# Kernel tuning notes

Hardware: AMD Instinct MI355X
Metric: run time of the kernel (lower is better)

Reference implementation:

```python
import jax, jax.numpy as jnp
from jax import lax
import numpy as np

B, W, V, E, H = 512, 40, 12000, 512, 512


def setup_inputs() -> dict:
    key = jax.random.key(0)
    ks = jax.random.split(key, 9)
    s = 0.05
    ques_vec = jax.random.randint(ks[0], (B, W), 0, V + 1)          # token ids, 0 = pad
    ques_len = jax.random.randint(ks[1], (B,), 1, W + 1)             # valid lengths in [1, W]
    lookup_W = jax.random.normal(ks[2], (E, V), jnp.float32) * s     # nn.Linear(vocab, emb).weight
    wih0 = jax.random.normal(ks[3], (2, 4 * H, E), jnp.float32) * s  # [dir, 4H, in]
    whh0 = jax.random.normal(ks[4], (2, 4 * H, H), jnp.float32) * s
    b0 = jax.random.normal(ks[5], (2, 2, 4 * H), jnp.float32) * s    # [dir, {b_ih,b_hh}, 4H]
    wih1 = jax.random.normal(ks[6], (2, 4 * H, 2 * H), jnp.float32) * s
    whh1 = jax.random.normal(ks[7], (2, 4 * H, H), jnp.float32) * s
    b1 = jax.random.normal(ks[8], (2, 2, 4 * H), jnp.float32) * s
    return {"ques_vec": ques_vec, "ques_len": ques_len, "lookup_W": lookup_W,
            "wih0": wih0, "whh0": whh0, "b0": b0,
            "wih1": wih1, "whh1": whh1, "b1": b1}


def _lstm_dir(x, wih, whh, b, reverse):
    # x: [B, T, D]; PyTorch gate order i, f, g, o
    Hc = whh.shape[1]
    xg = jnp.einsum('btd,gd->btg', x, wih) + b[0] + b[1]  # [B, T, 4H]
    xs = jnp.swapaxes(xg, 0, 1)                            # [T, B, 4H]
    if reverse:
        xs = xs[::-1]

    def step(carry, g_t):
        h, c = carry
        g = g_t + h @ whh.T
        i, f, gg, o = jnp.split(g, 4, axis=-1)
        c = jax.nn.sigmoid(f) * c + jax.nn.sigmoid(i) * jnp.tanh(gg)
        h = jax.nn.sigmoid(o) * jnp.tanh(c)
        return (h, c), h

    h0 = jnp.zeros((x.shape[0], Hc), x.dtype)
    _, hs = lax.scan(step, (h0, h0), xs)
    if reverse:
        hs = hs[::-1]
    return jnp.swapaxes(hs, 0, 1)  # [B, T, H]


def _bilstm(x, wih, whh, b):
    fwd = _lstm_dir(x, wih[0], whh[0], b[0], False)
    bwd = _lstm_dir(x, wih[1], whh[1], b[1], True)
    return jnp.concatenate([fwd, bwd], axis=-1)  # [B, T, 2H]


def reference(ques_vec, ques_len, lookup_W, wih0, whh0, b0, wih1, whh1, b1):
    # one-hot over vocab+1 with column 0 dropped == gather with id 0 -> zero vector
    table = jnp.concatenate([jnp.zeros((1, E), lookup_W.dtype), lookup_W.T], axis=0)  # [V+1, E]
    emb = jnp.tanh(table[ques_vec])          # [B, W, E] (dropout=0 -> identity)
    h = _bilstm(emb, wih0, whh0, b0)         # layer 0
    h = _bilstm(h, wih1, whh1, b1)           # layer 1 -> [B, W, 2H]
    # scatter-mask bmm == select hidden state at timestep ques_len-1
    idx = (ques_len - 1)[:, None, None]
    return jnp.take_along_axis(h, idx, axis=1).reshape(ques_vec.shape[0], -1)  # [B, 2H]
```

## Files before the change

### kernel.cpp

```cpp
#include <hip/hip_runtime.h>
#include <hip/hip_bf16.h>
#include <stdint.h>

#define NB 512
#define NW 40
#define NE 512
#define NH 512
#define NV 12000
#define G4 2048

typedef unsigned short u16;
typedef unsigned int u32;
typedef unsigned long long u64;
typedef __attribute__((ext_vector_type(8))) short short8;
typedef __attribute__((ext_vector_type(4))) float f32x4;

__device__ __forceinline__ unsigned short f2bf(float f) {
  unsigned int u = __float_as_uint(f);
  u += 0x7FFF + ((u >> 16) & 1);
  return (unsigned short)(u >> 16);
}
__device__ __forceinline__ float bf2f(unsigned short b) {
  return __uint_as_float(((unsigned int)b) << 16);
}
__device__ __forceinline__ float loadIn(const void* p, long i, int bf) {
  return bf ? bf2f(((const u16*)p)[i]) : ((const float*)p)[i];
}
__device__ __forceinline__ float fast_tanh(float x) {
  float ax = __builtin_fabsf(x);
  float t = 1.f - 2.f * __builtin_amdgcn_rcpf(__expf(ax + ax) + 1.f);
  return __builtin_copysignf(t, x);
}
__device__ __forceinline__ float sigm(float x) {
  return __builtin_amdgcn_rcpf(1.f + __expf(-x));
}

__global__ void detect_kernel(const u16* p, int* flag) {
  __shared__ int cnt;
  int i = threadIdx.x;
  if (i == 0) cnt = 0;
  __syncthreads();
  unsigned short u = p[2 * (i * 1001)];
  int e = (u >> 7) & 0xFF;
  if (e >= 100 && e <= 126) atomicAdd(&cnt, 1);
  __syncthreads();
  if (i == 0) *flag = (cnt >= 32) ? 1 : 0;
}

__global__ void table_kernel(const void* lookup, const int* flag, u16* tableT) {
  __shared__ float tile[64][65];
  int bf = *flag;
  int v0 = blockIdx.x * 64, e0 = blockIdx.y * 64;
  int tx = threadIdx.x, ty = threadIdx.y;
#pragma unroll
  for (int r = 0; r < 16; ++r) {
    int e = r * 4 + ty, v = tx;
    if (v0 + v < NV)
      tile[e][v] = tanhf(loadIn(lookup, (long)(e0 + e) * NV + v0 + v, bf));
  }
  __syncthreads();
#pragma unroll
  for (int r = 0; r < 16; ++r) {
    int v = r * 4 + ty, e = tx;
    if (v0 + v < NV)
      tableT[(long)(v0 + v) * NE + e0 + e] = f2bf(tile[e][v]);
  }
}

__global__ void pack_kernel(const void* wih0, const void* whh0, const void* b0,
                            const void* wih1, const void* whh1, const void* b1,
                            const int* flag, u16* Wc0, u16* Wc1, float* bsum,
                            u16* G) {
  const long N0 = 2L * G4 * 1024, N1 = 2L * G4 * 1536;
  const long NB2 = 2L * 2 * G4;
  long idx = (long)blockIdx.x * 256 + threadIdx.x;
  int bf = *flag;
  if (idx < N0) {
    int d = (int)(idx / (G4 * 1024));
    int rem = (int)(idx % (long)(G4 * 1024));
    int g = rem / 1024, k = rem % 1024;
    float v = (k < 512) ? loadIn(wih0, ((long)d * G4 + g) * 512 + k, bf)
                        : loadIn(whh0, ((long)d * G4 + g) * 512 + (k - 512), bf);
    Wc0[idx] = f2bf(v);
  } else if (idx < N0 + N1) {
    long i2 = idx - N0;
    int d = (int)(i2 / (G4 * 1536));
    int rem = (int)(i2 % (long)(G4 * 1536));
    int g = rem / 1536, k = rem % 1536;
    float v = (k < 1024) ? loadIn(wih1, ((long)d * G4 + g) * 1024 + k, bf)
                         : loadIn(whh1, ((long)d * G4 + g) * 512 + (k - 1024), bf);
    Wc1[i2] = f2bf(v);
  } else if (idx < N0 + N1 + NB2) {
    long i3 = idx - N0 - N1;
    int layer = (int)(i3 / (2 * G4));
    int d = (int)((i3 / G4) & 1);
    int g = (int)(i3 % G4);
    const void* bb = layer ? b1 : b0;
    float v = loadIn(bb, (long)d * 2 * G4 + g, bf) +
              loadIn(bb, (long)d * 2 * G4 + G4 + g, bf);
    bsum[i3] = v;
  } else if (idx < N0 + N1 + NB2 + 4096) {
    int n = (int)(idx - N0 - N1 - NB2);
    int d = n >> 11, loc = n & 2047;
    int colb = loc >> 7, rr = loc & 127;
    int jn = rr >> 2, g = rr & 3;
    int grow = g * 512 + colb * 32 + jn;
    float v = loadIn(b0, (long)d * 2 * G4 + grow, bf) +
              loadIn(b0, (long)d * 2 * G4 + G4 + grow, bf);
    G[n] = f2bf(v);
  }
}

__global__ void zero_bar(unsigned int* bar) {
  bar[blockIdx.x * 256 + threadIdx.x] = 0u;
}

__global__ __launch_bounds__(256, 3) void g_gemm(
    const u16* __restrict__ tableT, const u16* __restrict__ Wc,
    const float* __restrict__ bsumL, u16* __restrict__ G) {
  __shared__ __align__(16) char lds[32768];
  const int tid = threadIdx.x;
  const int lane = tid & 63, wv = tid >> 6;
  const int wm = wv & 1, wn = wv >> 1;
  const int col = lane & 15, quad = lane >> 4;
  const int bx = blockIdx.x >> 5;
  const int by = blockIdx.x & 31;
  const int tb0 = bx * 128;
  const int d = by >> 4, colb = by & 15, j0 = colb * 32;

  f32x4 zero = {0.f, 0.f, 0.f, 0.f};
  f32x4 acc[4][4];
#pragma unroll
  for (int i = 0; i < 4; ++i)
#pragma unroll
    for (int j = 0; j < 4; ++j) acc[i][j] = zero;

  for (int it = 0; it < 8; ++it) {
    int k0 = it << 6;
#pragma unroll
    for (int p = 0; p < 8; ++p) {
      int c = p * 256 + tid;
      const u16* gsrc;
      if (c < 1024) {
        int r = c >> 3, sl = c & 7;
        int kk = k0 + ((sl * 8) ^ ((r & 7) << 3));
        gsrc = tableT + (long)(tb0 + r) * 512 + kk;
      } else {
        int cb = c - 1024;
        int r = cb >> 3, sl = cb & 7;
        int kk = k0 + ((sl * 8) ^ ((r & 7) << 3));
        int grow = (r >> 5) * 512 + j0 + (r & 31);
        gsrc = Wc + ((long)d * G4 + grow) * 1024 + kk;
      }
      __builtin_amdgcn_global_load_lds(
          (const __attribute__((address_space(1))) void*)(const void*)gsrc,
          (__attribute__((address_space(3))) void*)(lds + p * 4096 + wv * 1024),
          16, 0, 0);
    }
    __syncthreads();
    const u16* As = (const u16*)lds;
    const u16* Bs = (const u16*)(lds + 16384);
#pragma unroll
    for (int ks = 0; ks < 2; ++ks) {
      short8 afr[4], bfr[4];
#pragma unroll
      for (int mf = 0; mf < 4; ++mf) {
        int rm = wm * 64 + mf * 16 + col;
        int sl = (ks * 32 + quad * 8) ^ ((rm & 7) << 3);
        afr[mf] = *(const short8*)(As + rm * 64 + sl);
      }
#pragma unroll
      for (int nf = 0; nf < 4; ++nf) {
        int br = wn * 64 + nf * 16 + col;
        int sl = (ks * 32 + quad * 8) ^ ((br & 7) << 3);
        bfr[nf] = *(const short8*)(Bs + br * 64 + sl);
      }
#pragma unroll
      for (int mf = 0; mf < 4; ++mf)
#pragma unroll
        for (int nf = 0; nf < 4; ++nf)
          acc[mf][nf] = __builtin_amdgcn_mfma_f32_16x16x32_bf16(
              afr[mf], bfr[nf], acc[mf][nf], 0, 0, 0);
    }
    __syncthreads();
  }

  float bias[4];
#pragma unroll
  for (int nf = 0; nf < 4; ++nf) {
    int n = wn * 64 + nf * 16 + col;
    bias[nf] = bsumL[d * G4 + (n >> 5) * 512 + j0 + (n & 31)];
  }
#pragma unroll
  for (int mf = 0; mf < 4; ++mf)
#pragma unroll
    for (int nf = 0; nf < 4; ++nf) {
      int n = wn * 64 + nf * 16 + col;
      int g = n >> 5, jn = n & 31;
#pragma unroll
      for (int r = 0; r < 4; ++r) {
        int m = wm * 64 + mf * 16 + quad * 4 + r;
        int v = tb0 + m;
        if (v < NV)
          G[(long)(v + 1) * 4096 + ((d * 16 + colb) << 7) + jn * 4 + g] =
              f2bf(acc[mf][nf][r] + bias[nf]);
      }
    }
}

__global__ __launch_bounds__(256, 3) void xg_gemm(
    const u16* __restrict__ X, int Kx, int Kfull, const u16* __restrict__ Wc,
    const float* __restrict__ bsumL, u16* __restrict__ xg) {
  __shared__ __align__(16) char lds[32768];
  const int tid = threadIdx.x;
  const int lane = tid & 63, wv = tid >> 6;
  const int wm = wv & 1, wn = wv >> 1;
  const int col = lane & 15, quad = lane >> 4;
  const int s = blockIdx.x >> 5, w = blockIdx.x & 31;
  const int bx = (s % 40) * 4 + (w & 3);
  const int by = (s / 40) * 8 + (w >> 2);
  const int tb0 = bx * 128;
  const int d = by >> 4, colb = by & 15, j0 = colb * 32;

  f32x4 zero = {0.f, 0.f, 0.f, 0.f};
  f32x4 acc[4][4];
#pragma unroll
  for (int i = 0; i < 4; ++i)
#pragma unroll
    for (int j = 0; j < 4; ++j) acc[i][j] = zero;

  const int iters = Kx >> 6;
  for (int it = 0; it < iters; ++it) {
    int k0 = it << 6;
#pragma unroll
    for (int p = 0; p < 8; ++p) {
      int c = p * 256 + tid;
      const u16* gsrc;
      if (c < 1024) {
        int r = c >> 3, sl = c & 7;
        int kk = k0 + ((sl * 8) ^ ((r & 7) << 3));
        gsrc = X + (long)(tb0 + r) * Kx + kk;
      } else {
        int cb = c - 1024;
        int r = cb >> 3, sl = cb & 7;
        int kk = k0 + ((sl * 8) ^ ((r & 7) << 3));
        int grow = (r >> 5) * 512 + j0 + (r & 31);
        gsrc = Wc + ((long)d * G4 + grow) * Kfull + kk;
      }
      __builtin_amdgcn_global_load_lds(
          (const __attribute__((address_space(1))) void*)(const void*)gsrc,
          (__attribute__((address_space(3))) void*)(lds + p * 4096 + wv * 1024),
          16, 0, 0);
    }
    __syncthreads();
    const u16* As = (const u16*)lds;
    const u16* Bs = (const u16*)(lds + 16384);
#pragma unroll
    for (int ks = 0; ks < 2; ++ks) {
      short8 afr[4], bfr[4];
#pragma unroll
      for (int mf = 0; mf < 4; ++mf) {
        int rm = wm * 64 + mf * 16 + col;
        int sl = (ks * 32 + quad * 8) ^ ((rm & 7) << 3);
        afr[mf] = *(const short8*)(As + rm * 64 + sl);
      }
#pragma unroll
      for (int nf = 0; nf < 4; ++nf) {
        int br = wn * 64 + nf * 16 + col;
        int sl = (ks * 32 + quad * 8) ^ ((br & 7) << 3);
        bfr[nf] = *(const short8*)(Bs + br * 64 + sl);
      }
#pragma unroll
      for (int mf = 0; mf < 4; ++mf)
#pragma unroll
        for (int nf = 0; nf < 4; ++nf)
          acc[mf][nf] = __builtin_amdgcn_mfma_f32_16x16x32_bf16(
              afr[mf], bfr[nf], acc[mf][nf], 0, 0, 0);
    }
    __syncthreads();
  }

  float bias[4];
#pragma unroll
  for (int nf = 0; nf < 4; ++nf) {
    int n = wn * 64 + nf * 16 + col;
    bias[nf] = bsumL[d * G4 + (n >> 5) * 512 + j0 + (n & 31)];
  }
#pragma unroll
  for (int mf = 0; mf < 4; ++mf)
#pragma unroll
    for (int nf = 0; nf < 4; ++nf) {
      int n = wn * 64 + nf * 16 + col;
      int g = n >> 5, jn = n & 31;
#pragma unroll
      for (int r = 0; r < 4; ++r) {
        int m = wm * 64 + mf * 16 + quad * 4 + r;
        int tb = tb0 + m, t = tb >> 9, b = tb & 511;
        long oi = ((((long)t * 2 + d) * 16 + colb) * 512 + b) * 128 + jn * 4 + g;
        xg[oi] = f2bf(acc[mf][nf][r] + bias[nf]);
      }
    }
}

__global__ __launch_bounds__(256, 1) void lstm_pers(
    const u16* __restrict__ xg, const int* __restrict__ qv,
    const u16* __restrict__ Wc, int Kfull, int Kx, u16* __restrict__ hbuf,
    u16* __restrict__ h0cat, void* __restrict__ outp,
    const int* __restrict__ qlen, const int* __restrict__ flag,
    unsigned int* bar, int layer) {
  __shared__ __align__(16) char lds[163840];
  const int tid = threadIdx.x;
  const int lane = tid & 63, wv = tid >> 6;
  const int wm = wv & 1, wn = wv >> 1;
  const int col = lane & 15, quad = lane >> 4;
  const int l = blockIdx.x;
  const int colid = l & 31, mi = l >> 5;
  const int colb = colid & 15, j0 = colb * 32, d = colid >> 4;
  const int m0 = mi * 64;
  const int gid = l >> 4;

#pragma unroll
  for (int p = 0; p < 24; ++p) {
    int c = p * 256 + tid;
    int cc = c >> 10, row = (c >> 3) & 127, sl = c & 7;
    int grow = (row >> 5) * 512 + j0 + (row & 31);
    int gk = Kx + 128 + cc * 64 + ((sl * 8) ^ ((row & 7) << 3));
    const u16* gsrc = Wc + ((long)d * G4 + grow) * Kfull + gk;
    __builtin_amdgcn_global_load_lds(
        (const __attribute__((address_space(1))) void*)(const void*)gsrc,
        (__attribute__((address_space(3))) void*)(lds + p * 4096 + wv * 1024),
        16, 0, 0);
  }
  const u16* WhhB = (const u16*)lds;
  char* hstg = lds + 98304;
  u16* hLDS = (u16*)hstg;

  short8 breg[4][4];
#pragma unroll
  for (int g = 0; g < 4; ++g) {
    int grow = g * 512 + j0 + wn * 16 + col;
    const u16* wp = Wc + ((long)d * G4 + grow) * Kfull + Kx;
#pragma unroll
    for (int c4 = 0; c4 < 4; ++c4)
      breg[g][c4] = *(const short8*)(wp + c4 * 32 + quad * 8);
  }

  float creg[2][4];
#pragma unroll
  for (int i = 0; i < 2; ++i)
#pragma unroll
    for (int r = 0; r < 4; ++r) creg[i][r] = 0.f;
  const int isbf = *flag;
  f32x4 zero = {0.f, 0.f, 0.f, 0.f};

  __syncthreads();

#pragma unroll 1
  for (int t = 0; t < NW; ++t) {
    const int tq = d ? (NW - 1 - t) : t;

    ushort4 xgv[2][4];
    if (layer == 0) {
#pragma unroll
      for (int mf = 0; mf < 2; ++mf)
#pragma unroll
        for (int r = 0; r < 4; ++r) {
          int m = wm * 32 + mf * 16 + quad * 4 + r;
          int q = qv[(m0 + m) * NW + tq];
          xgv[mf][r] = *(const ushort4*)(xg + (long)q * 4096 +
                                         ((d * 16 + colb) << 7) +
                                         (wn * 16 + col) * 4);
        }
    } else {
      const u16* xgt =
          xg + ((((long)tq * 2 + d) * 16 + colb) * 512 + m0) * 128;
#pragma unroll
      for (int mf = 0; mf < 2; ++mf)
#pragma unroll
        for (int r = 0; r < 4; ++r) {
          int m = wm * 32 + mf * 16 + quad * 4 + r;
          xgv[mf][r] = *(const ushort4*)(xgt + m * 128 + (wn * 16 + col) * 4);
        }
    }

    f32x4 acc[2][4];
#pragma unroll
    for (int i = 0; i < 2; ++i)
#pragma unroll
      for (int j = 0; j < 4; ++j) acc[i][j] = zero;

    if (t > 0) {
      if (wv == 0) {
        u32* sp = bar + gid * 16 + (lane & 15);
        while (__ballot((int)(__hip_atomic_load(sp, __ATOMIC_RELAXED,
                                                __HIP_MEMORY_SCOPE_AGENT) <
                              (u32)t)))
          __builtin_amdgcn_s_sleep(1);
      }
      __syncthreads();

      const u16* hp =
          hbuf + ((t - 1) & 1) * (2L * NB * NH) + ((long)d * NB + m0) * NH;
#pragma unroll
      for (int p = 0; p < 16; ++p) {
        int c = p * 256 + tid;
        int row = c >> 6, slot = c & 63;
        int kk = (slot >> 3) * 64 + (((slot & 7) * 8) ^ ((row & 7) << 3));
        const u16* gsrc = hp + (long)row * NH + kk;
        __builtin_amdgcn_global_load_lds(
            (const __attribute__((address_space(1))) void*)(const void*)gsrc,
            (__attribute__((address_space(3))) void*)(hstg + p * 4096 +
                                                      wv * 1024),
            16, 0, 16 );
      }
      __syncthreads();

      const u16* As = (const u16*)hstg;
#pragma unroll
      for (int ks = 0; ks < 16; ++ks) {
        const int ksub = ks * 32 + quad * 8;
        short8 afr[2];
#pragma unroll
        for (int mf = 0; mf < 2; ++mf) {
          int rm = wm * 32 + mf * 16 + col;
          afr[mf] = *(const short8*)(As + rm * 512 + (ksub & ~63) +
                                     ((ksub & 63) ^ ((rm & 7) << 3)));
        }
#pragma unroll
        for (int g = 0; g < 4; ++g) {
          short8 bfr;
          if (ks < 4) {
            bfr = breg[g][ks];
          } else {
            int br = g * 32 + wn * 16 + col;
            int kp = ksub - 128;
            bfr = *(const short8*)(WhhB + (kp >> 6) * 8192 + br * 64 +
                                   ((kp & 63) ^ ((br & 7) << 3)));
          }
#pragma unroll
          for (int mf = 0; mf < 2; ++mf)
            acc[mf][g] = __builtin_amdgcn_mfma_f32_16x16x32_bf16(
                afr[mf], bfr, acc[mf][g], 0, 0, 0);
        }
      }
      __syncthreads();
    }

#pragma unroll
    for (int mf = 0; mf < 2; ++mf)
#pragma unroll
      for (int r = 0; r < 4; ++r) {
        int m = wm * 32 + mf * 16 + quad * 4 + r;
        const u16* xv = (const u16*)&xgv[mf][r];
        float gi = acc[mf][0][r] + bf2f(xv[0]);
        float gf = acc[mf][1][r] + bf2f(xv[1]);
        float gg = acc[mf][2][r] + bf2f(xv[2]);
        float go = acc[mf][3][r] + bf2f(xv[3]);
        float si = sigm(gi);
        float sf = sigm(gf);
        float so = sigm(go);
        float cn = sf * creg[mf][r] + si * fast_tanh(gg);
        float h = so * fast_tanh(cn);
        creg[mf][r] = cn;
        hLDS[m * 32 + wn * 16 + col] = f2bf(h);
        if (layer == 1 && !isbf) {
          int bg = m0 + m;
          if (qlen[bg] - 1 == tq)
            ((float*)outp)[(long)bg * (2 * NH) + d * NH + j0 + wn * 16 + col] =
                h;
        }
      }
    __syncthreads();

    u16* hnxt = hbuf + (t & 1) * (2L * NB * NH);
    u32 hw[4];
    int bgp[4], jgp[4];
#pragma unroll
    for (int p = 0; p < 4; ++p) {
      int c = p * 256 + tid;
      int m = c >> 4, pr = c & 15;
      hw[p] = ((const u32*)hLDS)[m * 16 + pr];
      bgp[p] = m0 + m;
      jgp[p] = j0 + pr * 2;
      __hip_atomic_store(
          (u32*)(hnxt + ((long)d * NB + bgp[p]) * NH + jgp[p]), hw[p],
          __ATOMIC_RELAXED, __HIP_MEMORY_SCOPE_AGENT);
    }

    if (t < NW - 1) {
      __syncthreads();
      if (tid == 0)
        __hip_atomic_store(bar + gid * 16 + colb, (u32)(t + 1),
                           __ATOMIC_RELAXED, __HIP_MEMORY_SCOPE_AGENT);
    }

#pragma unroll
    for (int p = 0; p < 4; ++p) {
      if (layer == 0) {
        *(u32*)(h0cat + ((long)tq * NB + bgp[p]) * (2 * NH) + d * NH +
                jgp[p]) = hw[p];
      } else if (isbf && qlen[bgp[p]] - 1 == tq) {
        *(u32*)((u16*)outp + (long)bgp[p] * (2 * NH) + d * NH + jgp[p]) =
            hw[p];
      }
    }
  }
}

extern "C" void kernel_launch(void* const* d_in, const int* in_sizes, int n_in,
                              void* d_out, int out_size, void* d_ws,
                              size_t ws_size, hipStream_t stream) {
  const int* qv = (const int*)d_in[0];
  const int* ql = (const int*)d_in[1];
  const void* lookup = d_in[2];
  const void* wih0 = d_in[3];
  const void* whh0 = d_in[4];
  const void* b0 = d_in[5];
  const void* wih1 = d_in[6];
  const void* whh1 = d_in[7];
  const void* b1 = d_in[8];

  char* ws = (char*)d_ws;
  size_t off = 0;
  int* flag = (int*)ws;                 off += 256;
  unsigned int* bar = (unsigned int*)(ws + off); off += 8192;
  float* bsum = (float*)(ws + off);     off += 2L * 2 * G4 * 4;
  u16* Wc0 = (u16*)(ws + off);          off += 2L * G4 * 1024 * 2;
  u16* Wc1 = (u16*)(ws + off);          off += 2L * G4 * 1536 * 2;
  u16* hbuf = (u16*)(ws + off);         off += 2L * 2 * NB * NH * 2;
  u16* h0cat = (u16*)(ws + off);        off += (size_t)NW * NB * 2 * NH * 2;
  u16* xg = (u16*)(ws + off);           off += (size_t)NW * 2 * 16 * 512 * 128 * 2;
  u16* tableT = h0cat;
  u16* G = xg;

  detect_kernel<<<1, 64, 0, stream>>>((const u16*)lookup, flag);
  table_kernel<<<dim3(188, 8), dim3(64, 4), 0, stream>>>(lookup, flag, tableT);
  {
    long total = 2L * G4 * 1024 + 2L * G4 * 1536 + 2L * 2 * G4 + 4096;
    int blocks = (int)((total + 255) / 256);
    pack_kernel<<<blocks, 256, 0, stream>>>(wih0, whh0, b0, wih1, whh1, b1,
                                            flag, Wc0, Wc1, bsum, G);
  }

  g_gemm<<<94 * 32, 256, 0, stream>>>(tableT, Wc0, bsum, G);
  zero_bar<<<8, 256, 0, stream>>>(bar);
  lstm_pers<<<256, 256, 0, stream>>>(G, qv, Wc0, 1024, 512, hbuf, h0cat,
                                     d_out, ql, flag, bar, 0);
  xg_gemm<<<5120, 256, 0, stream>>>(h0cat, 1024, 1536, Wc1, bsum + 2 * G4, xg);
  zero_bar<<<8, 256, 0, stream>>>(bar);
  lstm_pers<<<256, 256, 0, stream>>>(xg, qv, Wc1, 1536, 1024, hbuf, h0cat,
                                     d_out, ql, flag, bar, 1);
}
```

Baseline: 832.5 us.

## Rewrite layer-1 input GEMM with 256x256 tiles and double-buffered LDS prefetch

The layer-1 input-projection GEMM now uses 512-thread blocks, each computing a 256x256 output tile. Global-to-LDS loads for the next K tile are double-buffered and interleaved with MFMA work, and s_setprio raises priority around the MFMA issue. Barrier zeroing is folded into pack_kernel, and each layer gets its own barrier region, which removes two tiny kernel launches. The cost is heavy LDS use (128KB) and one block per CU, which lowers occupancy. The loop is hardcoded to 16 K tiles, which assumes Kx=1024.

```diff
diff --git a/kernel.cpp b/kernel.cpp
--- a/kernel.cpp
+++ b/kernel.cpp
@@ -70,7 +70,7 @@
 __global__ void pack_kernel(const void* wih0, const void* whh0, const void* b0,
                             const void* wih1, const void* whh1, const void* b1,
                             const int* flag, u16* Wc0, u16* Wc1, float* bsum,
-                            u16* G) {
+                            u16* G, unsigned int* bar) {
   const long N0 = 2L * G4 * 1024, N1 = 2L * G4 * 1536;
   const long NB2 = 2L * 2 * G4;
   long idx = (long)blockIdx.x * 256 + threadIdx.x;
@@ -108,11 +108,9 @@
     float v = loadIn(b0, (long)d * 2 * G4 + grow, bf) +
               loadIn(b0, (long)d * 2 * G4 + G4 + grow, bf);
     G[n] = f2bf(v);
-  }
-}
-
-__global__ void zero_bar(unsigned int* bar) {
-  bar[blockIdx.x * 256 + threadIdx.x] = 0u;
+  } else if (idx < N0 + N1 + NB2 + 4096 + 512) {
+    bar[(int)(idx - N0 - N1 - NB2 - 4096)] = 0u;
+  }
 }
 
 __global__ __launch_bounds__(256, 3) void g_gemm(
@@ -208,98 +206,132 @@
     }
 }
 
-__global__ __launch_bounds__(256, 3) void xg_gemm(
+__global__ __launch_bounds__(512, 1) void xg_gemm(
     const u16* __restrict__ X, int Kx, int Kfull, const u16* __restrict__ Wc,
     const float* __restrict__ bsumL, u16* __restrict__ xg) {
-  __shared__ __align__(16) char lds[32768];
+  __shared__ __align__(16) char lds[131072];
   const int tid = threadIdx.x;
   const int lane = tid & 63, wv = tid >> 6;
-  const int wm = wv & 1, wn = wv >> 1;
+  const int wm = wv >> 2, wn = wv & 3;
   const int col = lane & 15, quad = lane >> 4;
-  const int s = blockIdx.x >> 5, w = blockIdx.x & 31;
-  const int bx = (s % 40) * 4 + (w & 3);
-  const int by = (s / 40) * 8 + (w >> 2);
-  const int tb0 = bx * 128;
-  const int d = by >> 4, colb = by & 15, j0 = colb * 32;
+  const int w = blockIdx.x & 15, s = blockIdx.x >> 4;
+  const int bx = (s % 20) * 4 + (w & 3);
+  const int by = (s / 20) * 4 + (w >> 2);
+  const int tb0 = bx * 256;
+  const int d = by >> 3;
 
   f32x4 zero = {0.f, 0.f, 0.f, 0.f};
-  f32x4 acc[4][4];
-#pragma unroll
-  for (int i = 0; i < 4; ++i)
+  f32x4 acc[8][4];
+#pragma unroll
+  for (int i = 0; i < 8; ++i)
 #pragma unroll
     for (int j = 0; j < 4; ++j) acc[i][j] = zero;
 
-  const int iters = Kx >> 6;
-  for (int it = 0; it < iters; ++it) {
-    int k0 = it << 6;
-#pragma unroll
-    for (int p = 0; p < 8; ++p) {
-      int c = p * 256 + tid;
+  const int nkt = Kx >> 6;
+
+  auto stage = [&](int kt, int j) {
+    char* dst = lds + (kt & 1) * 65536 + ((j >> 1) * 32768) + ((j & 1) * 16384);
+#pragma unroll
+    for (int i = 0; i < 2; ++i) {
+      int idx = i * 512 + tid;
+      int row = idx >> 3, sl = idx & 7;
+      int rr = (j & 1) * 128 + row;
+      int kk = kt * 64 + ((sl * 8) ^ ((rr & 7) << 3));
       const u16* gsrc;
-      if (c < 1024) {
-        int r = c >> 3, sl = c & 7;
-        int kk = k0 + ((sl * 8) ^ ((r & 7) << 3));
-        gsrc = X + (long)(tb0 + r) * Kx + kk;
+      if (j < 2) {
+        gsrc = X + (long)(tb0 + rr) * Kx + kk;
       } else {
-        int cb = c - 1024;
-        int r = cb >> 3, sl = cb & 7;
-        int kk = k0 + ((sl * 8) ^ ((r & 7) << 3));
-        int grow = (r >> 5) * 512 + j0 + (r & 31);
+        int n2 = (by & 7) * 256 + rr;
+        int grow = ((n2 & 127) >> 5) * 512 + (n2 >> 7) * 32 + (n2 & 31);
         gsrc = Wc + ((long)d * G4 + grow) * Kfull + kk;
       }
       __builtin_amdgcn_global_load_lds(
           (const __attribute__((address_space(1))) void*)(const void*)gsrc,
-          (__attribute__((address_space(3))) void*)(lds + p * 4096 + wv * 1024),
+          (__attribute__((address_space(3))) void*)(dst + i * 8192 + wv * 1024),
           16, 0, 0);
     }
-    __syncthreads();
-    const u16* As = (const u16*)lds;
-    const u16* Bs = (const u16*)(lds + 16384);
-#pragma unroll
-    for (int ks = 0; ks < 2; ++ks) {
-      short8 afr[4], bfr[4];
+  };
+
+#pragma unroll
+  for (int j = 0; j < 4; ++j) stage(0, j);
+
+#pragma unroll 1
+  for (int kt = 0; kt < 16; ++kt) {
+    if (kt + 1 < 16) {
+      stage(kt + 1, 0);
+      asm volatile("s_waitcnt vmcnt(2)" ::: "memory");
+    } else {
+      asm volatile("s_waitcnt vmcnt(0)" ::: "memory");
+    }
+    __builtin_amdgcn_sched_barrier(0);
+    __builtin_amdgcn_s_barrier();
+    __builtin_amdgcn_sched_barrier(0);
+
+    const u16* As = (const u16*)(lds + (kt & 1) * 65536);
+    const u16* Bs = As + 16384;
+
+#pragma unroll
+    for (int q = 0; q < 4; ++q) {
+      const int qr = q >> 1, qc = q & 1;
+      short8 afr[4][2], bfr[2][2];
 #pragma unroll
       for (int mf = 0; mf < 4; ++mf) {
-        int rm = wm * 64 + mf * 16 + col;
-        int sl = (ks * 32 + quad * 8) ^ ((rm & 7) << 3);
-        afr[mf] = *(const short8*)(As + rm * 64 + sl);
-      }
-#pragma unroll
-      for (int nf = 0; nf < 4; ++nf) {
-        int br = wn * 64 + nf * 16 + col;
-        int sl = (ks * 32 + quad * 8) ^ ((br & 7) << 3);
-        bfr[nf] = *(const short8*)(Bs + br * 64 + sl);
-      }
+        int rm = wm * 128 + qr * 64 + mf * 16 + col;
+#pragma unroll
+        for (int ks = 0; ks < 2; ++ks) {
+          int ksub = ks * 32 + quad * 8;
+          afr[mf][ks] =
+              *(const short8*)(As + rm * 64 + (ksub ^ ((rm & 7) << 3)));
+        }
+      }
+#pragma unroll
+      for (int nf = 0; nf < 2; ++nf) {
+        int bn = wn * 64 + qc * 32 + nf * 16 + col;
+#pragma unroll
+        for (int ks = 0; ks < 2; ++ks) {
+          int ksub = ks * 32 + quad * 8;
+          bfr[nf][ks] =
+              *(const short8*)(Bs + bn * 64 + (ksub ^ ((bn & 7) << 3)));
+        }
+      }
+      if (q > 0 && kt + 1 < 16) stage(kt + 1, q);
+      __builtin_amdgcn_s_setprio(1);
 #pragma unroll
       for (int mf = 0; mf < 4; ++mf)
 #pragma unroll
-        for (int nf = 0; nf < 4; ++nf)
-          acc[mf][nf] = __builtin_amdgcn_mfma_f32_16x16x32_bf16(
-              afr[mf], bfr[nf], acc[mf][nf], 0, 0, 0);
-    }
-    __syncthreads();
-  }
-
-  float bias[4];
+        for (int nf = 0; nf < 2; ++nf)
+#pragma unroll
+          for (int ks = 0; ks < 2; ++ks)
+            acc[qr * 4 + mf][qc * 2 + nf] =
+                __builtin_amdgcn_mfma_f32_16x16x32_bf16(
+                    afr[mf][ks], bfr[nf][ks], acc[qr * 4 + mf][qc * 2 + nf], 0,
+                    0, 0);
+      __builtin_amdgcn_s_setprio(0);
+      __builtin_amdgcn_sched_barrier(0);
+      __builtin_amdgcn_s_barrier();
+      __builtin_amdgcn_sched_barrier(0);
+    }
+  }
+
 #pragma unroll
   for (int nf = 0; nf < 4; ++nf) {
-    int n = wn * 64 + nf * 16 + col;
-    bias[nf] = bsumL[d * G4 + (n >> 5) * 512 + j0 + (n & 31)];
-  }
-#pragma unroll
-  for (int mf = 0; mf < 4; ++mf)
-#pragma unroll
-    for (int nf = 0; nf < 4; ++nf) {
-      int n = wn * 64 + nf * 16 + col;
-      int g = n >> 5, jn = n & 31;
+    int nc = wn * 64 + nf * 16 + col;
+    int n2 = (by & 7) * 256 + nc;
+    int colb = n2 >> 7, nq = n2 & 127;
+    int g = nq >> 5, jn = nq & 31;
+    float bias = bsumL[d * G4 + g * 512 + colb * 32 + jn];
+#pragma unroll
+    for (int mf = 0; mf < 8; ++mf) {
 #pragma unroll
       for (int r = 0; r < 4; ++r) {
-        int m = wm * 64 + mf * 16 + quad * 4 + r;
+        int m = wm * 128 + mf * 16 + quad * 4 + r;
         int tb = tb0 + m, t = tb >> 9, b = tb & 511;
-        long oi = ((((long)t * 2 + d) * 16 + colb) * 512 + b) * 128 + jn * 4 + g;
-        xg[oi] = f2bf(acc[mf][nf][r] + bias[nf]);
-      }
-    }
+        long oi =
+            ((((long)t * 2 + d) * 16 + colb) * 512 + b) * 128 + jn * 4 + g;
+        xg[oi] = f2bf(acc[mf][nf][r] + bias);
+      }
+    }
+  }
 }
 
 __global__ __launch_bounds__(256, 1) void lstm_pers(
@@ -536,18 +568,16 @@
   detect_kernel<<<1, 64, 0, stream>>>((const u16*)lookup, flag);
   table_kernel<<<dim3(188, 8), dim3(64, 4), 0, stream>>>(lookup, flag, tableT);
   {
-    long total = 2L * G4 * 1024 + 2L * G4 * 1536 + 2L * 2 * G4 + 4096;
+    long total = 2L * G4 * 1024 + 2L * G4 * 1536 + 2L * 2 * G4 + 4096 + 512;
     int blocks = (int)((total + 255) / 256);
     pack_kernel<<<blocks, 256, 0, stream>>>(wih0, whh0, b0, wih1, whh1, b1,
-                                            flag, Wc0, Wc1, bsum, G);
+                                            flag, Wc0, Wc1, bsum, G, bar);
   }
 
   g_gemm<<<94 * 32, 256, 0, stream>>>(tableT, Wc0, bsum, G);
-  zero_bar<<<8, 256, 0, stream>>>(bar);
   lstm_pers<<<256, 256, 0, stream>>>(G, qv, Wc0, 1024, 512, hbuf, h0cat,
                                      d_out, ql, flag, bar, 0);
-  xg_gemm<<<5120, 256, 0, stream>>>(h0cat, 1024, 1536, Wc1, bsum + 2 * G4, xg);
-  zero_bar<<<8, 256, 0, stream>>>(bar);
+  xg_gemm<<<1280, 512, 0, stream>>>(h0cat, 1024, 1536, Wc1, bsum + 2 * G4, xg);
   lstm_pers<<<256, 256, 0, stream>>>(xg, qv, Wc1, 1536, 1024, hbuf, h0cat,
-                                     d_out, ql, flag, bar, 1);
-}
+                                     d_out, ql, flag, bar + 256, 1);
+}
```

Result: slower. 920.5 us (+10.6%).
